# Kernel optimization log

Measured on AMD Instinct MI355X. Metric: run time of the kernel, lower is better.

The kernel has to match this reference:

```python
import jax, jax.numpy as jnp
import numpy as np

ALPHA_LO = float(np.exp(-1.0 / 5.0))   # 0.8187
ALPHA_HI = float(np.exp(-1.0 / 25.0))  # 0.9608
BN_EPS = 1e-5

B, T, D_IN, H = 32, 2000, 512, 512


def setup_inputs() -> dict:
    key = jax.random.key(0)
    ks = jax.random.split(key, 5)
    x = jax.random.normal(ks[0], (B, T, D_IN), dtype=jnp.float32)
    W = jax.random.normal(ks[1], (H, D_IN), dtype=jnp.float32) / np.sqrt(D_IN)
    b = jax.random.normal(ks[2], (H,), dtype=jnp.float32) * 0.01
    alpha = jax.random.uniform(ks[3], (H,), dtype=jnp.float32,
                               minval=ALPHA_LO, maxval=ALPHA_HI)
    gamma = jnp.ones((H,), dtype=jnp.float32)
    beta = jnp.zeros((H,), dtype=jnp.float32)
    ut0 = jax.random.uniform(ks[4], (B, H), dtype=jnp.float32)
    return {"x": x, "W": W, "b": b, "alpha": alpha,
            "gamma": gamma, "beta": beta, "ut0": ut0}


def reference(x, W, b, alpha, gamma, beta, ut0):
    # Linear: [B,T,Din] @ [Din,H] + b
    Wx = jnp.einsum("btd,hd->bth", x, W) + b
    # BatchNorm1d (training forward): stats over flattened (B*T) dim
    flat = Wx.reshape(-1, Wx.shape[-1])
    mean = flat.mean(axis=0)
    var = flat.var(axis=0)  # biased, as torch BN uses for normalization
    Wx = ((flat - mean) * jax.lax.rsqrt(var + BN_EPS) * gamma + beta).reshape(Wx.shape)
    # Readout cell: leaky integration + softmax accumulation over time
    a = jnp.clip(alpha, ALPHA_LO, ALPHA_HI)

    def step(carry, wxt):
        ut, acc = carry
        ut = a * ut + (1.0 - a) * wxt          # [B,H]
        acc = acc + jax.nn.softmax(ut, axis=1)
        return (ut, acc), None

    wx_t = jnp.transpose(Wx, (1, 0, 2))  # [T,B,H]
    (_, out), _ = jax.lax.scan(step, (ut0, jnp.zeros_like(ut0)), wx_t)
    return out[:, None, :]  # [B,1,H]
```

## Files before the change

### kernel.cpp

```cpp
#include <hip/hip_runtime.h>
#include <hip/hip_bf16.h>
#include <stdint.h>


namespace {
constexpr int kB = 32;
constexpr int kT = 2000;
constexpr int kD = 512;
constexpr int kH = 512;
constexpr int kM = kB * kT;
constexpr int kL = 20;
constexpr int kC = kT / kL;
constexpr float kALo = 0.81873075307798182f;
constexpr float kAHi = 0.96078943915232320f;

typedef __bf16 bf16x4 __attribute__((ext_vector_type(4)));
typedef __bf16 bf16x8 __attribute__((ext_vector_type(8)));
typedef float floatx16 __attribute__((ext_vector_type(16)));

__device__ __forceinline__ float bf2f(unsigned short u) {
  return __builtin_bit_cast(float, (unsigned)u << 16);
}
__device__ __forceinline__ float clipa(float a) {
  return fminf(fmaxf(a, kALo), kAHi);
}
__device__ __forceinline__ float pow20(float a) {
  const float a2 = a * a, a4 = a2 * a2, a5 = a4 * a;
  const float a10 = a5 * a5;
  return a10 * a10;
}
__device__ __forceinline__ void gld_lds16(const void* g, void* l) {
  __builtin_amdgcn_global_load_lds(
      (const __attribute__((address_space(1))) uint32_t*)g,
      (__attribute__((address_space(3))) uint32_t*)(uintptr_t)l, 16, 0, 0);
}

__global__ __launch_bounds__(256) void wcvt_k(const float* __restrict__ W,
                                              __bf16* __restrict__ Wbf) {
  const int t = blockIdx.x * 256 + threadIdx.x;
  const float4 a0 = ((const float4*)W)[t * 2];
  const float4 a1 = ((const float4*)W)[t * 2 + 1];
  bf16x8 v;
  v[0] = (__bf16)a0.x; v[1] = (__bf16)a0.y; v[2] = (__bf16)a0.z; v[3] = (__bf16)a0.w;
  v[4] = (__bf16)a1.x; v[5] = (__bf16)a1.y; v[6] = (__bf16)a1.z; v[7] = (__bf16)a1.w;
  const int h = t >> 6, k8 = t & 63;
  *(bf16x8*)(Wbf + ((size_t)k8 * 512 + h) * 8) = v;
}

__global__ __launch_bounds__(512, 2) void gemm_k(const float* __restrict__ X,
                                                 const __bf16* __restrict__ Wbf,
                                                 unsigned short* __restrict__ Wxb,
                                                 float* __restrict__ partial) {
  __shared__ alignas(16) __bf16 As2[4][65][8];
  __shared__ alignas(16) bf16x8 Bs2[2048];
  __shared__ float sred[2][kH];
  const int tid = threadIdx.x;
  const size_t row0 = (size_t)blockIdx.x * 64;
  const int w = tid >> 6, L = tid & 63;
  const int ct0 = w * 2;
  const int lhalf = L >> 5, l32 = L & 31;
  const int arow = tid >> 3, acol = (tid & 7) * 4;
  const int akq = acol >> 3, aoff = acol & 7;

  floatx16 acc[2][2] = {};
  const float* xbase = X + (row0 + arow) * kD + acol;
  float4 a_pre = *(const float4*)xbase;

#pragma unroll 1
  for (int s = 0; s < 16; ++s) {
    __syncthreads();
    bf16x4 av;
    av[0] = (__bf16)a_pre.x; av[1] = (__bf16)a_pre.y;
    av[2] = (__bf16)a_pre.z; av[3] = (__bf16)a_pre.w;
    *(bf16x4*)&As2[akq][arow][aoff] = av;
#pragma unroll
    for (int j = 0; j < 4; ++j) {
      const int ci = j * 512 + tid;
      gld_lds16(Wbf + ((size_t)s * 2048 + ci) * 8, (char*)&Bs2[0] + (size_t)ci * 16);
    }
    __syncthreads();
    if (s < 15) a_pre = *(const float4*)(xbase + (s + 1) * 32);
#pragma unroll
    for (int kh = 0; kh < 2; ++kh) {
      const int kq = kh * 2 + lhalf;
      const bf16x8 af0 = *(const bf16x8*)&As2[kq][l32][0];
      const bf16x8 af1 = *(const bf16x8*)&As2[kq][32 + l32][0];
      const bf16x8 b0 = Bs2[kq * 512 + ct0 * 32 + l32];
      const bf16x8 b1 = Bs2[kq * 512 + (ct0 + 1) * 32 + l32];
      acc[0][0] = __builtin_amdgcn_mfma_f32_32x32x16_bf16(af0, b0, acc[0][0], 0, 0, 0);
      acc[0][1] = __builtin_amdgcn_mfma_f32_32x32x16_bf16(af0, b1, acc[0][1], 0, 0, 0);
      acc[1][0] = __builtin_amdgcn_mfma_f32_32x32x16_bf16(af1, b0, acc[1][0], 0, 0, 0);
      acc[1][1] = __builtin_amdgcn_mfma_f32_32x32x16_bf16(af1, b1, acc[1][1], 0, 0, 0);
    }
  }

  __syncthreads();
  sred[0][tid] = 0.f;
  sred[1][tid] = 0.f;
  __syncthreads();
#pragma unroll
  for (int c = 0; c < 2; ++c) {
    float s = 0.f, q = 0.f;
#pragma unroll
    for (int rt = 0; rt < 2; ++rt) {
#pragma unroll
      for (int r = 0; r < 16; ++r) {
        const float v = acc[rt][c][r];
        s += v;
        q += v * v;
      }
    }
    s += __shfl_xor(s, 32);
    q += __shfl_xor(q, 32);
    if (lhalf == 0) {
      atomicAdd(&sred[0][(ct0 + c) * 32 + l32], s);
      atomicAdd(&sred[1][(ct0 + c) * 32 + l32], q);
    }
  }
#pragma unroll
  for (int rt = 0; rt < 2; ++rt) {
#pragma unroll
    for (int c = 0; c < 2; ++c) {
      const int col = (ct0 + c) * 32 + l32;
#pragma unroll
      for (int r = 0; r < 16; ++r) {
        const int row = rt * 32 + 4 * lhalf + (r & 3) + 8 * (r >> 2);
        const unsigned short u = __builtin_bit_cast(unsigned short, (__bf16)acc[rt][c][r]);
        const unsigned un = __shfl_down((unsigned)u, 1);
        if ((l32 & 1) == 0)
          *(unsigned*)(Wxb + (row0 + row) * (size_t)kH + col) = (unsigned)u | (un << 16);
      }
    }
  }
  __syncthreads();
  partial[(size_t)blockIdx.x * 1024 + tid] = sred[0][tid];
  partial[(size_t)blockIdx.x * 1024 + 512 + tid] = sred[1][tid];
}

__global__ __launch_bounds__(512) void red1_k(const float* __restrict__ partial,
                                              float* __restrict__ sums) {
  const int tid = threadIdx.x;
  const int r0 = blockIdx.x * 25;
  float s0 = 0.f, s1 = 0.f;
#pragma unroll 5
  for (int r = 0; r < 25; ++r) {
    s0 += partial[(size_t)(r0 + r) * 1024 + tid];
    s1 += partial[(size_t)(r0 + r) * 1024 + 512 + tid];
  }
  atomicAdd(&sums[tid], s0);
  atomicAdd(&sums[kH + tid], s1);
}

__global__ __launch_bounds__(512) void finalize_k(const float* __restrict__ sums,
                                                  const float* __restrict__ alpha,
                                                  const float* __restrict__ gamma,
                                                  const float* __restrict__ beta,
                                                  float* __restrict__ prm) {
  const int h = threadIdx.x;
  const float inv_n = 1.0f / (float)kM;
  const float mean = sums[h] * inv_n;
  const float var = sums[kH + h] * inv_n - mean * mean;
  const float sc = gamma[h] * rsqrtf(var + 1e-5f);
  const float sh = beta[h] - mean * sc;
  const float a = clipa(alpha[h]);
  prm[h] = sc;
  prm[kH + h] = sh;
  prm[2 * kH + h] = a;
  prm[3 * kH + h] = 1.0f - a;
  prm[4 * kH + h] = pow20(a);
}

__global__ __launch_bounds__(512) void agg_raw_k(const unsigned short* __restrict__ Wxb,
                                                 const float* __restrict__ alpha,
                                                 float* __restrict__ vbuf) {
  const int bc = blockIdx.x;
  const int b = bc / kC, c = bc % kC;
  const int h = threadIdx.x;
  const float a = clipa(alpha[h]);
  const float oma = 1.0f - a;
  const unsigned short* base = Wxb + ((size_t)b * kT + (size_t)c * kL) * kH + h;
  float v = 0.f;
#pragma unroll
  for (int i = 0; i < kL; ++i)
    v = a * v + oma * bf2f(base[(size_t)i * kH]);
  vbuf[(size_t)bc * kH + h] = v;
}

__global__ __launch_bounds__(512) void scan_k(const float* __restrict__ ut0,
                                              const float* __restrict__ alpha,
                                              const float* __restrict__ prm,
                                              float* __restrict__ vbuf) {
  const int b = blockIdx.x;
  const int h = threadIdx.x;
  const float a20 = pow20(clipa(alpha[h]));
  const float sc = prm[h];
  const float shc = prm[kH + h] * (1.0f - a20);
  float u = ut0[(size_t)b * kH + h];
  float vc[10];
#pragma unroll 1
  for (int cb = 0; cb < kC; cb += 10) {
#pragma unroll
    for (int j = 0; j < 10; ++j)
      vc[j] = vbuf[((size_t)b * kC + cb + j) * kH + h];
#pragma unroll
    for (int j = 0; j < 10; ++j) {
      vbuf[((size_t)b * kC + cb + j) * kH + h] = u;
      u = a20 * u + sc * vc[j] + shc;
    }
  }
}

__global__ __launch_bounds__(512) void soft_k(const unsigned short* __restrict__ Wxb,
                                              const float* __restrict__ prm,
                                              const float* __restrict__ ustart,
                                              float* __restrict__ accp) {
  __shared__ float part[kL][9];
  __shared__ float zinv[kL];
  const int bc = blockIdx.x;
  const int b = bc / kC, c = bc % kC;
  const int h = threadIdx.x;
  const int wv = h >> 6, lane = h & 63;
  const float sc = prm[h], sh = prm[kH + h];
  const float a = prm[2 * kH + h], oma = prm[3 * kH + h];
  float u = ustart[(size_t)bc * kH + h];
  const unsigned short* base = Wxb + ((size_t)b * kT + (size_t)c * kL) * kH + h;
  float e[kL];
#pragma unroll
  for (int i = 0; i < kL; ++i) {
    const float wvx = bf2f(base[(size_t)i * kH]) * sc + sh;
    u = a * u + oma * wvx;
    e[i] = __expf(u);
  }
#pragma unroll
  for (int i = 0; i < kL; ++i) {
    float s = e[i];
#pragma unroll
    for (int off = 32; off > 0; off >>= 1) s += __shfl_xor(s, off);
    if (lane == 0) part[i][wv] = s;
  }
  __syncthreads();
  if (h < kL) {
    float s = 0.f;
#pragma unroll
    for (int j = 0; j < 8; ++j) s += part[h][j];
    zinv[h] = 1.0f / s;
  }
  __syncthreads();
  float acc = 0.f;
#pragma unroll
  for (int i = 0; i < kL; ++i) acc += e[i] * zinv[i];
  accp[(size_t)bc * kH + h] = acc;
}

__global__ __launch_bounds__(512) void out_red_k(const float* __restrict__ accp,
                                                 float* __restrict__ out) {
  const int b = blockIdx.x;
  const int h = threadIdx.x;
  float s = 0.f;
#pragma unroll 4
  for (int c = 0; c < kC; ++c) s += accp[((size_t)b * kC + c) * kH + h];
  out[(size_t)b * kH + h] = s;
}

}

extern "C" void kernel_launch(void* const* d_in, const int* in_sizes, int n_in,
                              void* d_out, int out_size, void* d_ws, size_t ws_size,
                              hipStream_t stream) {
  const float* x = (const float*)d_in[0];
  const float* Wm = (const float*)d_in[1];
  const float* alpha = (const float*)d_in[3];
  const float* gamma = (const float*)d_in[4];
  const float* beta = (const float*)d_in[5];
  const float* ut0 = (const float*)d_in[6];
  float* out = (float*)d_out;

  float* wsp = (float*)d_ws;
  float* vbuf = wsp;
  float* accp = vbuf + (size_t)kB * kC * kH;
  float* partial = accp + (size_t)kB * kC * kH;
  float* sums = partial + (size_t)1000 * 1024;
  float* prm = sums + 2 * kH;
  __bf16* Wbf = (__bf16*)(prm + 5 * kH);
  unsigned short* Wxb = (unsigned short*)(Wbf + (size_t)kH * kD);

  hipMemsetAsync(sums, 0, 2 * kH * sizeof(float), stream);
  wcvt_k<<<128, 256, 0, stream>>>(Wm, Wbf);
  gemm_k<<<kM / 64, 512, 0, stream>>>(x, Wbf, Wxb, partial);
  agg_raw_k<<<kB * kC, 512, 0, stream>>>(Wxb, alpha, vbuf);
  red1_k<<<40, 512, 0, stream>>>(partial, sums);
  finalize_k<<<1, 512, 0, stream>>>(sums, alpha, gamma, beta, prm);
  scan_k<<<kB, 512, 0, stream>>>(ut0, alpha, prm, vbuf);
  soft_k<<<kB * kC, 512, 0, stream>>>(Wxb, prm, vbuf, accp);
  out_red_k<<<kB, 512, 0, stream>>>(accp, out);
}
```

Measured before the change: 308.9 us.

## Double-buffer GEMM LDS tiles and grow block M-tile to 128 rows

The projection GEMM now processes 128 rows per block instead of 64, so each wave computes a 4x2 grid of 32x32 MFMA tiles and every W tile loaded into LDS is reused across twice as many rows. The A and B shared-memory tiles are double-buffered, with the next K-step's W async copy and X conversion issued before the current step's MFMAs. Manual waitcnt and a raw barrier replace the two __syncthreads per step. This cuts W traffic and barrier stalls at the cost of more accumulator registers, more LDS, and half as many blocks. The partial-stats reduction is resized to match the 500 blocks.

```diff
diff --git a/kernel.cpp b/kernel.cpp
--- a/kernel.cpp
+++ b/kernel.cpp
@@ -9,6 +9,8 @@
 constexpr int kD = 512;
 constexpr int kH = 512;
 constexpr int kM = kB * kT;
+constexpr int kBM = 128;
+constexpr int kNB = kM / kBM;
 constexpr int kL = 20;
 constexpr int kC = kT / kL;
 constexpr float kALo = 0.81873075307798182f;
@@ -51,46 +53,80 @@
                                                  const __bf16* __restrict__ Wbf,
                                                  unsigned short* __restrict__ Wxb,
                                                  float* __restrict__ partial) {
-  __shared__ alignas(16) __bf16 As2[4][65][8];
-  __shared__ alignas(16) bf16x8 Bs2[2048];
+  __shared__ alignas(16) __bf16 As2[2][4][128][8];
+  __shared__ alignas(16) bf16x8 Bs2[2][2048];
   __shared__ float sred[2][kH];
   const int tid = threadIdx.x;
-  const size_t row0 = (size_t)blockIdx.x * 64;
+  const size_t row0 = (size_t)blockIdx.x * kBM;
   const int w = tid >> 6, L = tid & 63;
   const int ct0 = w * 2;
   const int lhalf = L >> 5, l32 = L & 31;
-  const int arow = tid >> 3, acol = (tid & 7) * 4;
-  const int akq = acol >> 3, aoff = acol & 7;
-
-  floatx16 acc[2][2] = {};
-  const float* xbase = X + (row0 + arow) * kD + acol;
-  float4 a_pre = *(const float4*)xbase;
+  const int arow = tid >> 2, akq = tid & 3;
+
+  floatx16 acc[4][2] = {};
+  const float* xptr = X + (row0 + arow) * kD + akq * 8;
+
+  float4 a0 = *(const float4*)xptr;
+  float4 a1 = *(const float4*)(xptr + 4);
+#pragma unroll
+  for (int j = 0; j < 4; ++j) {
+    const int ci = j * 512 + tid;
+    gld_lds16(Wbf + (size_t)ci * 8, (char*)&Bs2[0][0] + (size_t)ci * 16);
+  }
+  {
+    bf16x8 av;
+    av[0] = (__bf16)a0.x; av[1] = (__bf16)a0.y; av[2] = (__bf16)a0.z; av[3] = (__bf16)a0.w;
+    av[4] = (__bf16)a1.x; av[5] = (__bf16)a1.y; av[6] = (__bf16)a1.z; av[7] = (__bf16)a1.w;
+    *(bf16x8*)&As2[0][akq][arow][0] = av;
+  }
+  a0 = *(const float4*)(xptr + 32);
+  a1 = *(const float4*)(xptr + 36);
+  asm volatile("s_waitcnt vmcnt(2) lgkmcnt(0)" ::: "memory");
+  __builtin_amdgcn_s_barrier();
 
 #pragma unroll 1
   for (int s = 0; s < 16; ++s) {
-    __syncthreads();
-    bf16x4 av;
-    av[0] = (__bf16)a_pre.x; av[1] = (__bf16)a_pre.y;
-    av[2] = (__bf16)a_pre.z; av[3] = (__bf16)a_pre.w;
-    *(bf16x4*)&As2[akq][arow][aoff] = av;
-#pragma unroll
-    for (int j = 0; j < 4; ++j) {
-      const int ci = j * 512 + tid;
-      gld_lds16(Wbf + ((size_t)s * 2048 + ci) * 8, (char*)&Bs2[0] + (size_t)ci * 16);
-    }
-    __syncthreads();
-    if (s < 15) a_pre = *(const float4*)(xbase + (s + 1) * 32);
+    const int buf = s & 1;
+    if (s < 15) {
+#pragma unroll
+      for (int j = 0; j < 4; ++j) {
+        const int ci = j * 512 + tid;
+        gld_lds16(Wbf + ((size_t)(s + 1) * 2048 + ci) * 8,
+                  (char*)&Bs2[buf ^ 1][0] + (size_t)ci * 16);
+      }
+      bf16x8 av;
+      av[0] = (__bf16)a0.x; av[1] = (__bf16)a0.y; av[2] = (__bf16)a0.z; av[3] = (__bf16)a0.w;
+      av[4] = (__bf16)a1.x; av[5] = (__bf16)a1.y; av[6] = (__bf16)a1.z; av[7] = (__bf16)a1.w;
+      *(bf16x8*)&As2[buf ^ 1][akq][arow][0] = av;
+      if (s < 14) {
+        a0 = *(const float4*)(xptr + (s + 2) * 32);
+        a1 = *(const float4*)(xptr + (s + 2) * 32 + 4);
+      }
+    }
 #pragma unroll
     for (int kh = 0; kh < 2; ++kh) {
       const int kq = kh * 2 + lhalf;
-      const bf16x8 af0 = *(const bf16x8*)&As2[kq][l32][0];
-      const bf16x8 af1 = *(const bf16x8*)&As2[kq][32 + l32][0];
-      const bf16x8 b0 = Bs2[kq * 512 + ct0 * 32 + l32];
-      const bf16x8 b1 = Bs2[kq * 512 + (ct0 + 1) * 32 + l32];
+      const bf16x8 af0 = *(const bf16x8*)&As2[buf][kq][l32][0];
+      const bf16x8 af1 = *(const bf16x8*)&As2[buf][kq][32 + l32][0];
+      const bf16x8 af2 = *(const bf16x8*)&As2[buf][kq][64 + l32][0];
+      const bf16x8 af3 = *(const bf16x8*)&As2[buf][kq][96 + l32][0];
+      const bf16x8 b0 = Bs2[buf][kq * 512 + ct0 * 32 + l32];
+      const bf16x8 b1 = Bs2[buf][kq * 512 + (ct0 + 1) * 32 + l32];
       acc[0][0] = __builtin_amdgcn_mfma_f32_32x32x16_bf16(af0, b0, acc[0][0], 0, 0, 0);
       acc[0][1] = __builtin_amdgcn_mfma_f32_32x32x16_bf16(af0, b1, acc[0][1], 0, 0, 0);
       acc[1][0] = __builtin_amdgcn_mfma_f32_32x32x16_bf16(af1, b0, acc[1][0], 0, 0, 0);
       acc[1][1] = __builtin_amdgcn_mfma_f32_32x32x16_bf16(af1, b1, acc[1][1], 0, 0, 0);
+      acc[2][0] = __builtin_amdgcn_mfma_f32_32x32x16_bf16(af2, b0, acc[2][0], 0, 0, 0);
+      acc[2][1] = __builtin_amdgcn_mfma_f32_32x32x16_bf16(af2, b1, acc[2][1], 0, 0, 0);
+      acc[3][0] = __builtin_amdgcn_mfma_f32_32x32x16_bf16(af3, b0, acc[3][0], 0, 0, 0);
+      acc[3][1] = __builtin_amdgcn_mfma_f32_32x32x16_bf16(af3, b1, acc[3][1], 0, 0, 0);
+    }
+    if (s < 15) {
+      if (s < 14)
+        asm volatile("s_waitcnt vmcnt(2) lgkmcnt(0)" ::: "memory");
+      else
+        asm volatile("s_waitcnt vmcnt(0) lgkmcnt(0)" ::: "memory");
+      __builtin_amdgcn_s_barrier();
     }
   }
 
@@ -102,7 +138,7 @@
   for (int c = 0; c < 2; ++c) {
     float s = 0.f, q = 0.f;
 #pragma unroll
-    for (int rt = 0; rt < 2; ++rt) {
+    for (int rt = 0; rt < 4; ++rt) {
 #pragma unroll
       for (int r = 0; r < 16; ++r) {
         const float v = acc[rt][c][r];
@@ -118,7 +154,7 @@
     }
   }
 #pragma unroll
-  for (int rt = 0; rt < 2; ++rt) {
+  for (int rt = 0; rt < 4; ++rt) {
 #pragma unroll
     for (int c = 0; c < 2; ++c) {
       const int col = (ct0 + c) * 32 + l32;
@@ -140,10 +176,10 @@
 __global__ __launch_bounds__(512) void red1_k(const float* __restrict__ partial,
                                               float* __restrict__ sums) {
   const int tid = threadIdx.x;
-  const int r0 = blockIdx.x * 25;
+  const int r0 = blockIdx.x * 20;
   float s0 = 0.f, s1 = 0.f;
 #pragma unroll 5
-  for (int r = 0; r < 25; ++r) {
+  for (int r = 0; r < 20; ++r) {
     s0 += partial[(size_t)(r0 + r) * 1024 + tid];
     s1 += partial[(size_t)(r0 + r) * 1024 + 512 + tid];
   }
@@ -286,9 +322,9 @@
 
   hipMemsetAsync(sums, 0, 2 * kH * sizeof(float), stream);
   wcvt_k<<<128, 256, 0, stream>>>(Wm, Wbf);
-  gemm_k<<<kM / 64, 512, 0, stream>>>(x, Wbf, Wxb, partial);
+  gemm_k<<<kNB, 512, 0, stream>>>(x, Wbf, Wxb, partial);
   agg_raw_k<<<kB * kC, 512, 0, stream>>>(Wxb, alpha, vbuf);
-  red1_k<<<40, 512, 0, stream>>>(partial, sums);
+  red1_k<<<25, 512, 0, stream>>>(partial, sums);
   finalize_k<<<1, 512, 0, stream>>>(sums, alpha, gamma, beta, prm);
   scan_k<<<kB, 512, 0, stream>>>(ut0, alpha, prm, vbuf);
   soft_k<<<kB * kC, 512, 0, stream>>>(Wxb, prm, vbuf, accp);
```

Result: faster. 301.1 us (-2.5%).
